# Performance work log

Hardware: AMD Instinct MI355X
Metric: run time of the kernel (lower is better)

Reference implementation:

```python
import jax, jax.numpy as jnp
import numpy as np

N_NODES = 50000
N_EDGES = 800000
F_IN, HID, CLS = 128, 128, 64
DELTA = 3.0


def setup_inputs() -> dict:
    key = jax.random.key(0)
    ks = jax.random.split(key, 16)
    x = jax.random.normal(ks[0], (N_NODES, F_IN), jnp.float32)
    src = jax.random.randint(ks[1], (N_EDGES,), 0, N_NODES, jnp.int64)
    dst = jax.random.randint(ks[2], (N_EDGES,), 0, N_NODES, jnp.int64)
    dims = [(F_IN, HID), (HID, HID), (HID, CLS)]
    inp = {"x": x, "src": src, "dst": dst}
    k = 3
    for i, (din, dout) in enumerate(dims):
        inp[f"M{i}_w"] = jax.random.normal(ks[k], (2 * din, din), jnp.float32) * 0.05; k += 1
        inp[f"M{i}_b"] = jnp.zeros((din,), jnp.float32)
        inp[f"U{i}_w"] = jax.random.normal(ks[k], (10 * din, dout), jnp.float32) * 0.05; k += 1
        inp[f"U{i}_b"] = jnp.zeros((dout,), jnp.float32)
    return inp


def _pna_layer(h, src, dst, deg, logd, Mw, Mb, Uw, Ub):
    # message: per-edge linear on concat(src feat, dst feat)  [E, 2*din] @ [2*din, din]
    msg = jnp.concatenate([h[src], h[dst]], axis=1) @ Mw + Mb  # [E, din]
    n = h.shape[0]
    cnt = deg[:, None]                                          # [N, 1]
    has_nbr = cnt > 0
    mean = jax.ops.segment_sum(msg, dst, num_segments=n) / jnp.maximum(cnt, 1.0)
    mn = jax.ops.segment_min(msg, dst, num_segments=n)
    mx = jax.ops.segment_max(msg, dst, num_segments=n)
    mn = jnp.where(has_nbr, mn, 0.0)
    mx = jnp.where(has_nbr, mx, 0.0)
    agg = jnp.concatenate([mean, mn, mx], axis=1)               # [N, 3*din]
    amp = (logd / DELTA)[:, None]                               # amplification scaler
    att = (DELTA / jnp.maximum(logd, 1e-6))[:, None]            # attenuation scaler
    h_neigh = jnp.concatenate([agg, agg * amp, agg * att], axis=1)  # [N, 9*din]
    return jnp.concatenate([h, h_neigh], axis=1) @ Uw + Ub      # [N, dout]


def reference(x, src, dst, M0_w, M0_b, U0_w, U0_b, M1_w, M1_b, U1_w, U1_b, M2_w, M2_b, U2_w, U2_b):
    n = x.shape[0]
    deg = jax.ops.segment_sum(jnp.ones_like(dst, dtype=x.dtype), dst, num_segments=n)
    logd = jnp.log(deg + 1.0)
    params = [(M0_w, M0_b, U0_w, U0_b), (M1_w, M1_b, U1_w, U1_b), (M2_w, M2_b, U2_w, U2_b)]
    h = x
    for i, (Mw, Mb, Uw, Ub) in enumerate(params):
        h = _pna_layer(h, src, dst, deg, logd, Mw, Mb, Uw, Ub)
        if i != len(params) - 1:
            h = jax.nn.relu(h)
    return h
```

## Files before the change

kernel.cpp:

```cpp
#include <hip/hip_runtime.h>
#include <math.h>

#define N_NODES 50000
#define N_EDGES 800000
#define DIN 128
#define NB_SCAN ((N_NODES + 255) / 256)

typedef unsigned short u16;
typedef unsigned int u32;
typedef short short8 __attribute__((ext_vector_type(8)));
typedef float f32x4 __attribute__((ext_vector_type(4)));

__device__ __forceinline__ u16 f2bf(float x) {
  u32 u = __float_as_uint(x);
  u32 r = (u + 0x7FFFu + ((u >> 16) & 1u)) >> 16;
  return (u16)r;
}
__device__ __forceinline__ float bf2f(u16 h) { return __uint_as_float(((u32)h) << 16); }
__device__ __forceinline__ u32 pack2bf(float x, float y) {
  return (u32)f2bf(x) | ((u32)f2bf(y) << 16);
}

__device__ __forceinline__ f32x4 mfma_bf16(short8 a, short8 b, f32x4 c) {
  return __builtin_amdgcn_mfma_f32_16x16x32_bf16(a, b, c, 0, 0, 0);
}

__device__ __forceinline__ void g2l16(const void* g, void* l) {
  __builtin_amdgcn_global_load_lds(
      (const __attribute__((address_space(1))) u32*)g,
      (__attribute__((address_space(3))) u32*)l, 16, 0, 0);
}

#define SWZ(row, byt) ((row) * 128 + ((byt) ^ (((row) & 7) << 4)))


__global__ void k_deg(const int* __restrict__ dst, int* __restrict__ deg) {
  int e = blockIdx.x * blockDim.x + threadIdx.x;
  if (e < N_EDGES) atomicAdd(&deg[dst[e]], 1);
}

__global__ void k_scan_local(const int* __restrict__ deg, int* __restrict__ excl,
                             int* __restrict__ bsum) {
  __shared__ int sm[256];
  int tid = threadIdx.x;
  int i = blockIdx.x * 256 + tid;
  int v = (i < N_NODES) ? deg[i] : 0;
  sm[tid] = v;
  __syncthreads();
  for (int off = 1; off < 256; off <<= 1) {
    int t = (tid >= off) ? sm[tid - off] : 0;
    __syncthreads();
    sm[tid] += t;
    __syncthreads();
  }
  if (i < N_NODES) excl[i] = sm[tid] - v;
  if (tid == 255) bsum[blockIdx.x] = sm[255];
}

__global__ void k_scan_bsum(const int* __restrict__ bsum, int* __restrict__ boff,
                            int* __restrict__ row_off) {
  __shared__ int sm[256];
  int tid = threadIdx.x;
  int v = (tid < NB_SCAN) ? bsum[tid] : 0;
  sm[tid] = v;
  __syncthreads();
  for (int off = 1; off < 256; off <<= 1) {
    int t = (tid >= off) ? sm[tid - off] : 0;
    __syncthreads();
    sm[tid] += t;
    __syncthreads();
  }
  if (tid < NB_SCAN) boff[tid] = sm[tid] - v;
  if (tid == 255) row_off[N_NODES] = sm[255];
}

__global__ void k_scan_add(const int* __restrict__ excl, const int* __restrict__ boff,
                           int* __restrict__ row_off) {
  int i = blockIdx.x * 256 + threadIdx.x;
  if (i < N_NODES) row_off[i] = excl[i] + boff[i >> 8];
}

__global__ void k_node_init(const int* __restrict__ deg, const int* __restrict__ row_off,
                            int* __restrict__ cursor, float* __restrict__ amp,
                            float* __restrict__ att) {
  int v = blockIdx.x * blockDim.x + threadIdx.x;
  if (v >= N_NODES) return;
  cursor[v] = row_off[v];
  float d = (float)deg[v];
  float logd = logf(d + 1.0f);
  amp[v] = logd / 3.0f;
  att[v] = 3.0f / fmaxf(logd, 1e-6f);
}

__global__ void k_fill(const int* __restrict__ src, const int* __restrict__ dst,
                       int* __restrict__ cursor, int* __restrict__ nbr) {
  int e = blockIdx.x * blockDim.x + threadIdx.x;
  if (e >= N_EDGES) return;
  int slot = atomicAdd(&cursor[dst[e]], 1);
  nbr[slot] = src[e];
}


__global__ void k_prep_ab(const float* __restrict__ Mw, const float* __restrict__ Mb,
                          u16* __restrict__ Th, u16* __restrict__ Tl,
                          float* __restrict__ bias_ab) {
  int j = blockIdx.x;
  int k = threadIdx.x;
  float w = (j < 128) ? Mw[k * 128 + j] : Mw[(128 + k) * 128 + (j - 128)];
  u16 hi = f2bf(w);
  u16 lo = f2bf(w - bf2f(hi));
  Th[j * 128 + k] = hi;
  Tl[j * 128 + k] = lo;
  if (k == 0) bias_ab[j] = (j < 128) ? 0.f : Mb[j - 128];
}

__global__ void k_prep_u(const float* __restrict__ Uw, u16* __restrict__ Th,
                         u16* __restrict__ Tl, int Nout) {
  int k = blockIdx.x * 256 + threadIdx.x;
  int j = blockIdx.y;
  int p = blockIdx.z;
  if (p > 0 && k < 128) return;
  int srow = (p == 0) ? k : 512 + 384 * (p - 1) + (k - 128);
  float w = Uw[(size_t)srow * Nout + j];
  u16 hi = f2bf(w);
  u16 lo = f2bf(w - bf2f(hi));
  size_t idx = ((size_t)p * Nout + j) * 512 + k;
  Th[idx] = hi;
  Tl[idx] = lo;
}


__global__ void k_pack_x(const float* __restrict__ x, u16* __restrict__ Xh,
                         u16* __restrict__ Xl) {
  int i = blockIdx.x * 256 + threadIdx.x;
  if (i >= N_NODES * DIN) return;
  int g = i >> 7, c = i & 127;
  float v = x[i];
  u16 hi = f2bf(v);
  Xh[(size_t)g * 512 + c] = hi;
  Xl[(size_t)g * 128 + c] = f2bf(v - bf2f(hi));
}


__global__ __launch_bounds__(256, 3) void k_ab_gemm(
    const u16* __restrict__ Xh, const u16* __restrict__ Xl,
    const u16* __restrict__ WTh, const u16* __restrict__ WTl,
    const float* __restrict__ bias, u16* __restrict__ ABa, float* __restrict__ ABb) {
  __shared__ __align__(16) u16 Ah[128 * 64];
  __shared__ __align__(16) u16 Al[128 * 64];
  __shared__ __align__(16) u16 Bh[64 * 64];
  __shared__ __align__(16) u16 Bl[64 * 64];

  const int tid = threadIdx.x;
  const int row0 = blockIdx.x * 128;
  const int col0 = blockIdx.y * 64;
  const int lane = tid & 63;
  const int wave = tid >> 6;
  const int wrow = (wave >> 1) * 64;
  const int wcol = (wave & 1) * 32;

  f32x4 acc[4][2];
  const f32x4 zero4 = {0.f, 0.f, 0.f, 0.f};
#pragma unroll
  for (int i = 0; i < 4; ++i)
#pragma unroll
    for (int n = 0; n < 2; ++n) acc[i][n] = zero4;

  for (int k0 = 0; k0 < 128; k0 += 64) {
    __syncthreads();
#pragma unroll
    for (int r = 0; r < 4; ++r) {
      int op = r * 256 + tid;
      int m = op >> 3, ch = op & 7;
      int chx = ch ^ (m & 7);
      int g = row0 + m;
      if (g >= N_NODES) g = N_NODES - 1;
      g2l16(Xh + (size_t)g * 512 + k0 + chx * 8, (char*)Ah + op * 16);
      g2l16(Xl + (size_t)g * 128 + k0 + chx * 8, (char*)Al + op * 16);
    }
#pragma unroll
    for (int r = 0; r < 2; ++r) {
      int op = r * 256 + tid;
      int c = op >> 3, sl = op & 7;
      int slx = sl ^ (c & 7);
      g2l16(WTh + (size_t)(col0 + c) * 128 + k0 + slx * 8, (char*)Bh + op * 16);
      g2l16(WTl + (size_t)(col0 + c) * 128 + k0 + slx * 8, (char*)Bl + op * 16);
    }
    __syncthreads();
#pragma unroll
    for (int kk = 0; kk < 2; ++kk) {
      const int kb = kk * 64 + (lane >> 4) * 16;
      short8 a_h[4], a_l[4];
#pragma unroll
      for (int i = 0; i < 4; ++i) {
        int rr = wrow + i * 16 + (lane & 15);
        a_h[i] = *(const short8*)((const char*)Ah + SWZ(rr, kb));
        a_l[i] = *(const short8*)((const char*)Al + SWZ(rr, kb));
      }
#pragma unroll
      for (int n = 0; n < 2; ++n) {
        int cc = wcol + n * 16 + (lane & 15);
        short8 b_h = *(const short8*)((const char*)Bh + SWZ(cc, kb));
        short8 b_l = *(const short8*)((const char*)Bl + SWZ(cc, kb));
#pragma unroll
        for (int i = 0; i < 4; ++i) {
          acc[i][n] = mfma_bf16(a_h[i], b_h, acc[i][n]);
          acc[i][n] = mfma_bf16(a_h[i], b_l, acc[i][n]);
          acc[i][n] = mfma_bf16(a_l[i], b_h, acc[i][n]);
        }
      }
    }
  }
#pragma unroll
  for (int i = 0; i < 4; ++i) {
#pragma unroll
    for (int n = 0; n < 2; ++n) {
      int gr0 = row0 + wrow + i * 16 + (lane >> 4) * 4;
      int gc = col0 + wcol + n * 16 + (lane & 15);
#pragma unroll
      for (int q = 0; q < 4; ++q) {
        int gr = gr0 + q;
        if (gr >= N_NODES) continue;
        float v = acc[i][n][q];
        if (gc < 128) ABa[(size_t)gr * 128 + gc] = f2bf(v);
        else ABb[(size_t)gr * 128 + (gc - 128)] = v + bias[gc];
      }
    }
  }
}


template <int BN, int LAST>
__global__ __launch_bounds__(256, 3) void k_u_fused(
    const u16* __restrict__ Xh, const u16* __restrict__ Xl,
    const u16* __restrict__ UTh, const u16* __restrict__ UTl,
    const float* __restrict__ Ub, const float* __restrict__ amp,
    const float* __restrict__ att, u16* __restrict__ XhW, u16* __restrict__ XlW,
    float* __restrict__ outF, int Nout) {
  constexpr int NREP = BN / 32;
  constexpr int BE = BN * 64;
  constexpr int L1E = 16384 + 2 * BE;
  constexpr int L2E = 8192 + 4 * BE;
  constexpr int LDSE = (L1E > L2E) ? L1E : L2E;
  __shared__ __align__(16) u16 LDS[LDSE];
  u16* Ah  = LDS;
  u16* Al  = LDS + 8192;
  u16* B0h = LDS + 16384;
  u16* B0l = LDS + 16384 + BE;
  u16* B1h = LDS + 8192;
  u16* B1l = LDS + 8192 + BE;
  u16* B2h = LDS + 8192 + 2 * BE;
  u16* B2l = LDS + 8192 + 3 * BE;

  const int tid = threadIdx.x;
  const int row0 = blockIdx.x * 128;
  const int col0 = blockIdx.y * BN;
  const int lane = tid & 63;
  const int wave = tid >> 6;
  const int wrow = (wave >> 1) * 64;
  const int wcol = (wave & 1) * (BN / 2);

  const u16* U0h = UTh + (size_t)col0 * 512;
  const u16* U0l = UTl + (size_t)col0 * 512;
  const u16* U1h = UTh + (size_t)(Nout + col0) * 512;
  const u16* U1l = UTl + (size_t)(Nout + col0) * 512;
  const u16* U2h = UTh + (size_t)(2 * Nout + col0) * 512;
  const u16* U2l = UTl + (size_t)(2 * Nout + col0) * 512;

  f32x4 acc_t[4][NREP], acc_p1[4][NREP], acc_p2[4][NREP];
  const f32x4 zero4 = {0.f, 0.f, 0.f, 0.f};
#pragma unroll
  for (int i = 0; i < 4; ++i)
#pragma unroll
    for (int n = 0; n < NREP; ++n) {
      acc_t[i][n] = zero4; acc_p1[i][n] = zero4; acc_p2[i][n] = zero4;
    }

  for (int k0 = 0; k0 < 512; k0 += 64) {
    const bool hstep = (k0 < 128);
    __syncthreads();
#pragma unroll
    for (int r = 0; r < 4; ++r) {
      int op = r * 256 + tid;
      int m = op >> 3, ch = op & 7;
      int chx = ch ^ (m & 7);
      int g = row0 + m;
      if (g >= N_NODES) g = N_NODES - 1;
      g2l16(Xh + (size_t)g * 512 + k0 + chx * 8, (char*)Ah + op * 16);
      if (hstep) g2l16(Xl + (size_t)g * 128 + k0 + chx * 8, (char*)Al + op * 16);
    }
#pragma unroll
    for (int r = 0; r < NREP; ++r) {
      int op = r * 256 + tid;
      int c = op >> 3, sl = op & 7;
      int slx = sl ^ (c & 7);
      g2l16(U0h + (size_t)c * 512 + k0 + slx * 8, (char*)B0h + op * 16);
      g2l16(U0l + (size_t)c * 512 + k0 + slx * 8, (char*)B0l + op * 16);
    }
    __syncthreads();
#pragma unroll
    for (int kk = 0; kk < 2; ++kk) {
      const int kb = kk * 64 + (lane >> 4) * 16;
      short8 a_h[4], a_l[4];
#pragma unroll
      for (int i = 0; i < 4; ++i) {
        int rr = wrow + i * 16 + (lane & 15);
        a_h[i] = *(const short8*)((const char*)Ah + SWZ(rr, kb));
        if (hstep) a_l[i] = *(const short8*)((const char*)Al + SWZ(rr, kb));
      }
#pragma unroll
      for (int n = 0; n < NREP; ++n) {
        int cc = wcol + n * 16 + (lane & 15);
        short8 b_h = *(const short8*)((const char*)B0h + SWZ(cc, kb));
        short8 b_l = *(const short8*)((const char*)B0l + SWZ(cc, kb));
#pragma unroll
        for (int i = 0; i < 4; ++i) {
          acc_t[i][n] = mfma_bf16(a_h[i], b_h, acc_t[i][n]);
          acc_t[i][n] = mfma_bf16(a_h[i], b_l, acc_t[i][n]);
          if (hstep) acc_t[i][n] = mfma_bf16(a_l[i], b_h, acc_t[i][n]);
        }
      }
    }
  }

  for (int k0 = 128; k0 < 512; k0 += 64) {
    __syncthreads();
#pragma unroll
    for (int r = 0; r < 4; ++r) {
      int op = r * 256 + tid;
      int m = op >> 3, ch = op & 7;
      int chx = ch ^ (m & 7);
      int g = row0 + m;
      if (g >= N_NODES) g = N_NODES - 1;
      g2l16(Xh + (size_t)g * 512 + k0 + chx * 8, (char*)Ah + op * 16);
    }
#pragma unroll
    for (int r = 0; r < NREP; ++r) {
      int op = r * 256 + tid;
      int c = op >> 3, sl = op & 7;
      int slx = sl ^ (c & 7);
      size_t so = (size_t)c * 512 + k0 + slx * 8;
      g2l16(U1h + so, (char*)B1h + op * 16);
      g2l16(U1l + so, (char*)B1l + op * 16);
      g2l16(U2h + so, (char*)B2h + op * 16);
      g2l16(U2l + so, (char*)B2l + op * 16);
    }
    __syncthreads();
#pragma unroll
    for (int kk = 0; kk < 2; ++kk) {
      const int kb = kk * 64 + (lane >> 4) * 16;
      short8 a_h[4];
#pragma unroll
      for (int i = 0; i < 4; ++i) {
        int rr = wrow + i * 16 + (lane & 15);
        a_h[i] = *(const short8*)((const char*)Ah + SWZ(rr, kb));
      }
#pragma unroll
      for (int n = 0; n < NREP; ++n) {
        int cc = wcol + n * 16 + (lane & 15);
        short8 b1h = *(const short8*)((const char*)B1h + SWZ(cc, kb));
        short8 b1l = *(const short8*)((const char*)B1l + SWZ(cc, kb));
        short8 b2h = *(const short8*)((const char*)B2h + SWZ(cc, kb));
        short8 b2l = *(const short8*)((const char*)B2l + SWZ(cc, kb));
#pragma unroll
        for (int i = 0; i < 4; ++i) {
          acc_p1[i][n] = mfma_bf16(a_h[i], b1h, acc_p1[i][n]);
          acc_p1[i][n] = mfma_bf16(a_h[i], b1l, acc_p1[i][n]);
          acc_p2[i][n] = mfma_bf16(a_h[i], b2h, acc_p2[i][n]);
          acc_p2[i][n] = mfma_bf16(a_h[i], b2l, acc_p2[i][n]);
        }
      }
    }
  }

#pragma unroll
  for (int i = 0; i < 4; ++i) {
    int gr0 = row0 + wrow + i * 16 + (lane >> 4) * 4;
    f32x4 a1 = *(const f32x4*)(amp + gr0);
    f32x4 a2 = *(const f32x4*)(att + gr0);
#pragma unroll
    for (int n = 0; n < NREP; ++n) {
      int gc = col0 + wcol + n * 16 + (lane & 15);
      float b = Ub[gc];
#pragma unroll
      for (int q = 0; q < 4; ++q) {
        int gr = gr0 + q;
        if (gr >= N_NODES) continue;
        float v = acc_t[i][n][q] + a1[q] * acc_p1[i][n][q] + a2[q] * acc_p2[i][n][q] + b;
        if (LAST) {
          outF[(size_t)gr * 64 + gc] = v;
        } else {
          float t = fmaxf(v, 0.f);
          u16 hi = f2bf(t);
          XhW[(size_t)gr * 512 + gc] = hi;
          XlW[(size_t)gr * 128 + gc] = f2bf(t - bf2f(hi));
        }
      }
    }
  }
}


__global__ __launch_bounds__(256) void k_agg(const u16* __restrict__ ABa,
                                             const float* __restrict__ ABb,
                                             const int* __restrict__ row_off,
                                             const int* __restrict__ nbr,
                                             u16* __restrict__ XhDst) {
  int v = blockIdx.x * 4 + (threadIdx.x >> 6);
  int lane = threadIdx.x & 63;
  if (v >= N_NODES) return;
  int beg = row_off[v], end = row_off[v + 1];
  const u32* A32 = (const u32*)ABa;
  float sx = 0.f, sy = 0.f;
  float mnx = 3.4e38f, mny = 3.4e38f;
  float mxx = -3.4e38f, mxy = -3.4e38f;
  int i = beg;
#define ACC(w)                                              \
  {                                                         \
    float ax = bf2f((u16)(w)), ay = bf2f((u16)((w) >> 16)); \
    sx += ax; sy += ay;                                     \
    mnx = fminf(mnx, ax); mny = fminf(mny, ay);             \
    mxx = fmaxf(mxx, ax); mxy = fmaxf(mxy, ay);             \
  }
  for (; i + 4 <= end; i += 4) {
    int s0 = nbr[i], s1 = nbr[i + 1], s2 = nbr[i + 2], s3 = nbr[i + 3];
    u32 w0 = A32[(size_t)s0 * 64 + lane];
    u32 w1 = A32[(size_t)s1 * 64 + lane];
    u32 w2 = A32[(size_t)s2 * 64 + lane];
    u32 w3 = A32[(size_t)s3 * 64 + lane];
    ACC(w0) ACC(w1) ACC(w2) ACC(w3)
  }
  for (; i < end; ++i) {
    u32 w = A32[(size_t)nbr[i] * 64 + lane];
    ACC(w)
  }
#undef ACC
  int d = end - beg;
  int c = lane * 2;
  float2 b = *(const float2*)&ABb[(size_t)v * 128 + c];
  float mex, mey, mix, miy, max_, may_;
  if (d > 0) {
    float inv = 1.f / (float)d;
    mex = sx * inv + b.x; mey = sy * inv + b.y;
    mix = mnx + b.x; miy = mny + b.y;
    max_ = mxx + b.x; may_ = mxy + b.y;
  } else {
    mex = mey = mix = miy = max_ = may_ = 0.f;
  }
  u16* xr = XhDst + (size_t)v * 512 + 128 + c;
  *(u32*)(xr)       = pack2bf(mex, mey);
  *(u32*)(xr + 128) = pack2bf(mix, miy);
  *(u32*)(xr + 256) = pack2bf(max_, may_);
}


extern "C" void kernel_launch(void* const* d_in, const int* in_sizes, int n_in,
                              void* d_out, int out_size, void* d_ws, size_t ws_size,
                              hipStream_t stream) {
  const float* x   = (const float*)d_in[0];
  const int*   src = (const int*)d_in[1];
  const int*   dst = (const int*)d_in[2];
  const float* Mw[3] = {(const float*)d_in[3], (const float*)d_in[7],  (const float*)d_in[11]};
  const float* Mb[3] = {(const float*)d_in[4], (const float*)d_in[8],  (const float*)d_in[12]};
  const float* Uw[3] = {(const float*)d_in[5], (const float*)d_in[9],  (const float*)d_in[13]};
  const float* Ub[3] = {(const float*)d_in[6], (const float*)d_in[10], (const float*)d_in[14]};
  float* out = (float*)d_out;

  char* ws = (char*)d_ws;
  size_t o = 0;
  auto alloc = [&](size_t bytes) -> char* {
    o = (o + 255) & ~(size_t)255;
    char* p = ws + o;
    o += bytes;
    return p;
  };
  int*   deg_i   = (int*)alloc((size_t)N_NODES * 4);
  int*   row_off = (int*)alloc((size_t)(N_NODES + 1) * 4);
  int*   excl    = (int*)alloc((size_t)N_NODES * 4);
  int*   bsum    = (int*)alloc((size_t)NB_SCAN * 4);
  int*   boff    = (int*)alloc((size_t)NB_SCAN * 4);
  int*   cursor  = (int*)alloc((size_t)N_NODES * 4);
  float* amp     = (float*)alloc((size_t)N_NODES * 4);
  float* att     = (float*)alloc((size_t)N_NODES * 4);
  int*   nbr     = (int*)alloc((size_t)N_EDGES * 4);
  u16*   Xh0     = (u16*)alloc((size_t)N_NODES * 512 * 2);
  u16*   Xl0     = (u16*)alloc((size_t)N_NODES * 128 * 2);
  u16*   Xh1     = (u16*)alloc((size_t)N_NODES * 512 * 2);
  u16*   Xl1     = (u16*)alloc((size_t)N_NODES * 128 * 2);
  u16*   ABa     = (u16*)alloc((size_t)N_NODES * 128 * 2);
  float* ABb     = (float*)alloc((size_t)N_NODES * 128 * 4);
  u16*   WabTh[3]; u16* WabTl[3]; float* bias_ab[3];
  u16*   UTh[3];   u16* UTl[3];
  const int Nouts[3] = {128, 128, 64};
  for (int L = 0; L < 3; ++L) {
    WabTh[L] = (u16*)alloc((size_t)256 * 128 * 2);
    WabTl[L] = (u16*)alloc((size_t)256 * 128 * 2);
    bias_ab[L] = (float*)alloc(256 * 4);
    UTh[L] = (u16*)alloc((size_t)3 * Nouts[L] * 512 * 2);
    UTl[L] = (u16*)alloc((size_t)3 * Nouts[L] * 512 * 2);
  }

  hipMemsetAsync(deg_i, 0, (size_t)N_NODES * 4, stream);
  k_deg<<<(N_EDGES + 255) / 256, 256, 0, stream>>>(dst, deg_i);
  k_scan_local<<<NB_SCAN, 256, 0, stream>>>(deg_i, excl, bsum);
  k_scan_bsum<<<1, 256, 0, stream>>>(bsum, boff, row_off);
  k_scan_add<<<NB_SCAN, 256, 0, stream>>>(excl, boff, row_off);
  k_node_init<<<(N_NODES + 255) / 256, 256, 0, stream>>>(deg_i, row_off, cursor, amp, att);
  k_fill<<<(N_EDGES + 255) / 256, 256, 0, stream>>>(src, dst, cursor, nbr);

  for (int L = 0; L < 3; ++L) {
    k_prep_ab<<<256, 128, 0, stream>>>(Mw[L], Mb[L], WabTh[L], WabTl[L], bias_ab[L]);
    k_prep_u<<<dim3(2, Nouts[L], 3), 256, 0, stream>>>(Uw[L], UTh[L], UTl[L], Nouts[L]);
  }
  k_pack_x<<<(N_NODES * DIN + 255) / 256, 256, 0, stream>>>(x, Xh0, Xl0);

  const int MT = (N_NODES + 127) / 128;
  u16* XhIn[3] = {Xh0, Xh1, Xh0};
  u16* XlIn[3] = {Xl0, Xl1, Xl0};
  u16* XhOut[3] = {Xh1, Xh0, nullptr};
  u16* XlOut[3] = {Xl1, Xl0, nullptr};

  for (int L = 0; L < 3; ++L) {
    k_ab_gemm<<<dim3(MT, 4), 256, 0, stream>>>(XhIn[L], XlIn[L], WabTh[L], WabTl[L],
                                               bias_ab[L], ABa, ABb);
    k_agg<<<(N_NODES + 3) / 4, 256, 0, stream>>>(ABa, ABb, row_off, nbr, XhIn[L]);
    if (L < 2) {
      k_u_fused<64, 0><<<dim3(MT, 2), 256, 0, stream>>>(
          XhIn[L], XlIn[L], UTh[L], UTl[L], Ub[L], amp, att,
          XhOut[L], XlOut[L], nullptr, Nouts[L]);
    } else {
      k_u_fused<32, 1><<<dim3(MT, 2), 256, 0, stream>>>(
          XhIn[L], XlIn[L], UTh[L], UTl[L], Ub[L], amp, att,
          nullptr, nullptr, out, Nouts[L]);
    }
  }
}
```

Before: 601.2 us.

## Swap grid axes, merge U-GEMM k-loops, and vectorize aggregation per 16-lane node group

Result: faster. 568.4 us (-5.5%).

```diff
diff --git a/kernel.cpp b/kernel.cpp
--- a/kernel.cpp
+++ b/kernel.cpp
@@ -152,8 +152,8 @@
   __shared__ __align__(16) u16 Bl[64 * 64];
 
   const int tid = threadIdx.x;
-  const int row0 = blockIdx.x * 128;
-  const int col0 = blockIdx.y * 64;
+  const int row0 = blockIdx.y * 128;
+  const int col0 = blockIdx.x * 64;
   const int lane = tid & 63;
   const int wave = tid >> 6;
   const int wrow = (wave >> 1) * 64;
@@ -231,7 +231,7 @@
 
 
 template <int BN, int LAST>
-__global__ __launch_bounds__(256, 3) void k_u_fused(
+__global__ __launch_bounds__(256, 2) void k_u_fused(
     const u16* __restrict__ Xh, const u16* __restrict__ Xl,
     const u16* __restrict__ UTh, const u16* __restrict__ UTl,
     const float* __restrict__ Ub, const float* __restrict__ amp,
@@ -239,22 +239,20 @@
     float* __restrict__ outF, int Nout) {
   constexpr int NREP = BN / 32;
   constexpr int BE = BN * 64;
-  constexpr int L1E = 16384 + 2 * BE;
-  constexpr int L2E = 8192 + 4 * BE;
-  constexpr int LDSE = (L1E > L2E) ? L1E : L2E;
+  constexpr int LDSE = 8192 + 2 * BE + ((4 * BE > 8192) ? 4 * BE : 8192);
   __shared__ __align__(16) u16 LDS[LDSE];
   u16* Ah  = LDS;
-  u16* Al  = LDS + 8192;
-  u16* B0h = LDS + 16384;
-  u16* B0l = LDS + 16384 + BE;
-  u16* B1h = LDS + 8192;
-  u16* B1l = LDS + 8192 + BE;
-  u16* B2h = LDS + 8192 + 2 * BE;
-  u16* B2l = LDS + 8192 + 3 * BE;
+  u16* B0h = LDS + 8192;
+  u16* B0l = LDS + 8192 + BE;
+  u16* B1h = LDS + 8192 + 2 * BE;
+  u16* B1l = LDS + 8192 + 3 * BE;
+  u16* B2h = LDS + 8192 + 4 * BE;
+  u16* B2l = LDS + 8192 + 5 * BE;
+  u16* Al  = LDS + 8192 + 2 * BE;
 
   const int tid = threadIdx.x;
-  const int row0 = blockIdx.x * 128;
-  const int col0 = blockIdx.y * BN;
+  const int row0 = blockIdx.y * 128;
+  const int col0 = blockIdx.x * BN;
   const int lane = tid & 63;
   const int wave = tid >> 6;
   const int wrow = (wave >> 1) * 64;
@@ -294,8 +292,15 @@
       int op = r * 256 + tid;
       int c = op >> 3, sl = op & 7;
       int slx = sl ^ (c & 7);
-      g2l16(U0h + (size_t)c * 512 + k0 + slx * 8, (char*)B0h + op * 16);
-      g2l16(U0l + (size_t)c * 512 + k0 + slx * 8, (char*)B0l + op * 16);
+      size_t so = (size_t)c * 512 + k0 + slx * 8;
+      g2l16(U0h + so, (char*)B0h + op * 16);
+      g2l16(U0l + so, (char*)B0l + op * 16);
+      if (!hstep) {
+        g2l16(U1h + so, (char*)B1h + op * 16);
+        g2l16(U1l + so, (char*)B1l + op * 16);
+        g2l16(U2h + so, (char*)B2h + op * 16);
+        g2l16(U2l + so, (char*)B2l + op * 16);
+      }
     }
     __syncthreads();
 #pragma unroll
@@ -311,63 +316,26 @@
 #pragma unroll
       for (int n = 0; n < NREP; ++n) {
         int cc = wcol + n * 16 + (lane & 15);
-        short8 b_h = *(const short8*)((const char*)B0h + SWZ(cc, kb));
-        short8 b_l = *(const short8*)((const char*)B0l + SWZ(cc, kb));
+        short8 b0h = *(const short8*)((const char*)B0h + SWZ(cc, kb));
+        short8 b0l = *(const short8*)((const char*)B0l + SWZ(cc, kb));
 #pragma unroll
         for (int i = 0; i < 4; ++i) {
-          acc_t[i][n] = mfma_bf16(a_h[i], b_h, acc_t[i][n]);
-          acc_t[i][n] = mfma_bf16(a_h[i], b_l, acc_t[i][n]);
-          if (hstep) acc_t[i][n] = mfma_bf16(a_l[i], b_h, acc_t[i][n]);
+          acc_t[i][n] = mfma_bf16(a_h[i], b0h, acc_t[i][n]);
+          acc_t[i][n] = mfma_bf16(a_h[i], b0l, acc_t[i][n]);
+          if (hstep) acc_t[i][n] = mfma_bf16(a_l[i], b0h, acc_t[i][n]);
         }
-      }
-    }
-  }
-
-  for (int k0 = 128; k0 < 512; k0 += 64) {
-    __syncthreads();
-#pragma unroll
-    for (int r = 0; r < 4; ++r) {
-      int op = r * 256 + tid;
-      int m = op >> 3, ch = op & 7;
-      int chx = ch ^ (m & 7);
-      int g = row0 + m;
-      if (g >= N_NODES) g = N_NODES - 1;
-      g2l16(Xh + (size_t)g * 512 + k0 + chx * 8, (char*)Ah + op * 16);
-    }
-#pragma unroll
-    for (int r = 0; r < NREP; ++r) {
-      int op = r * 256 + tid;
-      int c = op >> 3, sl = op & 7;
-      int slx = sl ^ (c & 7);
-      size_t so = (size_t)c * 512 + k0 + slx * 8;
-      g2l16(U1h + so, (char*)B1h + op * 16);
-      g2l16(U1l + so, (char*)B1l + op * 16);
-      g2l16(U2h + so, (char*)B2h + op * 16);
-      g2l16(U2l + so, (char*)B2l + op * 16);
-    }
-    __syncthreads();
-#pragma unroll
-    for (int kk = 0; kk < 2; ++kk) {
-      const int kb = kk * 64 + (lane >> 4) * 16;
-      short8 a_h[4];
-#pragma unroll
-      for (int i = 0; i < 4; ++i) {
-        int rr = wrow + i * 16 + (lane & 15);
-        a_h[i] = *(const short8*)((const char*)Ah + SWZ(rr, kb));
-      }
-#pragma unroll
-      for (int n = 0; n < NREP; ++n) {
-        int cc = wcol + n * 16 + (lane & 15);
-        short8 b1h = *(const short8*)((const char*)B1h + SWZ(cc, kb));
-        short8 b1l = *(const short8*)((const char*)B1l + SWZ(cc, kb));
-        short8 b2h = *(const short8*)((const char*)B2h + SWZ(cc, kb));
-        short8 b2l = *(const short8*)((const char*)B2l + SWZ(cc, kb));
-#pragma unroll
-        for (int i = 0; i < 4; ++i) {
-          acc_p1[i][n] = mfma_bf16(a_h[i], b1h, acc_p1[i][n]);
-          acc_p1[i][n] = mfma_bf16(a_h[i], b1l, acc_p1[i][n]);
-          acc_p2[i][n] = mfma_bf16(a_h[i], b2h, acc_p2[i][n]);
-          acc_p2[i][n] = mfma_bf16(a_h[i], b2l, acc_p2[i][n]);
+        if (!hstep) {
+          short8 b1h = *(const short8*)((const char*)B1h + SWZ(cc, kb));
+          short8 b1l = *(const short8*)((const char*)B1l + SWZ(cc, kb));
+          short8 b2h = *(const short8*)((const char*)B2h + SWZ(cc, kb));
+          short8 b2l = *(const short8*)((const char*)B2l + SWZ(cc, kb));
+#pragma unroll
+          for (int i = 0; i < 4; ++i) {
+            acc_p1[i][n] = mfma_bf16(a_h[i], b1h, acc_p1[i][n]);
+            acc_p1[i][n] = mfma_bf16(a_h[i], b1l, acc_p1[i][n]);
+            acc_p2[i][n] = mfma_bf16(a_h[i], b2h, acc_p2[i][n]);
+            acc_p2[i][n] = mfma_bf16(a_h[i], b2l, acc_p2[i][n]);
+          }
         }
       }
     }
@@ -406,51 +374,55 @@
                                              const int* __restrict__ row_off,
                                              const int* __restrict__ nbr,
                                              u16* __restrict__ XhDst) {
-  int v = blockIdx.x * 4 + (threadIdx.x >> 6);
+  int wv = blockIdx.x * 4 + (threadIdx.x >> 6);
   int lane = threadIdx.x & 63;
+  int grp = lane >> 4;
+  int sub = lane & 15;
+  int v = wv * 4 + grp;
   if (v >= N_NODES) return;
   int beg = row_off[v], end = row_off[v + 1];
-  const u32* A32 = (const u32*)ABa;
-  float sx = 0.f, sy = 0.f;
-  float mnx = 3.4e38f, mny = 3.4e38f;
-  float mxx = -3.4e38f, mxy = -3.4e38f;
-  int i = beg;
-#define ACC(w)                                              \
-  {                                                         \
-    float ax = bf2f((u16)(w)), ay = bf2f((u16)((w) >> 16)); \
-    sx += ax; sy += ay;                                     \
-    mnx = fminf(mnx, ax); mny = fminf(mny, ay);             \
-    mxx = fmaxf(mxx, ax); mxy = fmaxf(mxy, ay);             \
-  }
-  for (; i + 4 <= end; i += 4) {
-    int s0 = nbr[i], s1 = nbr[i + 1], s2 = nbr[i + 2], s3 = nbr[i + 3];
-    u32 w0 = A32[(size_t)s0 * 64 + lane];
-    u32 w1 = A32[(size_t)s1 * 64 + lane];
-    u32 w2 = A32[(size_t)s2 * 64 + lane];
-    u32 w3 = A32[(size_t)s3 * 64 + lane];
-    ACC(w0) ACC(w1) ACC(w2) ACC(w3)
-  }
-  for (; i < end; ++i) {
-    u32 w = A32[(size_t)nbr[i] * 64 + lane];
-    ACC(w)
-  }
-#undef ACC
+  const uint4* A16 = (const uint4*)ABa;
+  float s[8], mn[8], mx[8];
+#pragma unroll
+  for (int c = 0; c < 8; ++c) { s[c] = 0.f; mn[c] = 3.4e38f; mx[c] = -3.4e38f; }
+  for (int i = beg; i < end; ++i) {
+    int sidx = nbr[i];
+    uint4 w = A16[(size_t)sidx * 16 + sub];
+    u32 ww[4] = {w.x, w.y, w.z, w.w};
+#pragma unroll
+    for (int j = 0; j < 4; ++j) {
+      float ax = bf2f((u16)ww[j]), ay = bf2f((u16)(ww[j] >> 16));
+      s[2 * j] += ax; s[2 * j + 1] += ay;
+      mn[2 * j] = fminf(mn[2 * j], ax); mn[2 * j + 1] = fminf(mn[2 * j + 1], ay);
+      mx[2 * j] = fmaxf(mx[2 * j], ax); mx[2 * j + 1] = fmaxf(mx[2 * j + 1], ay);
+    }
+  }
   int d = end - beg;
-  int c = lane * 2;
-  float2 b = *(const float2*)&ABb[(size_t)v * 128 + c];
-  float mex, mey, mix, miy, max_, may_;
+  float bb[8];
+  {
+    f32x4 b0 = *(const f32x4*)(ABb + (size_t)v * 128 + sub * 8);
+    f32x4 b1 = *(const f32x4*)(ABb + (size_t)v * 128 + sub * 8 + 4);
+#pragma unroll
+    for (int c = 0; c < 4; ++c) { bb[c] = b0[c]; bb[4 + c] = b1[c]; }
+  }
+  uint4 wm, wn, wx;
+  u32* pm = &wm.x; u32* pn = &wn.x; u32* px = &wx.x;
   if (d > 0) {
     float inv = 1.f / (float)d;
-    mex = sx * inv + b.x; mey = sy * inv + b.y;
-    mix = mnx + b.x; miy = mny + b.y;
-    max_ = mxx + b.x; may_ = mxy + b.y;
+#pragma unroll
+    for (int j = 0; j < 4; ++j) {
+      pm[j] = pack2bf(s[2 * j] * inv + bb[2 * j], s[2 * j + 1] * inv + bb[2 * j + 1]);
+      pn[j] = pack2bf(mn[2 * j] + bb[2 * j], mn[2 * j + 1] + bb[2 * j + 1]);
+      px[j] = pack2bf(mx[2 * j] + bb[2 * j], mx[2 * j + 1] + bb[2 * j + 1]);
+    }
   } else {
-    mex = mey = mix = miy = max_ = may_ = 0.f;
-  }
-  u16* xr = XhDst + (size_t)v * 512 + 128 + c;
-  *(u32*)(xr)       = pack2bf(mex, mey);
-  *(u32*)(xr + 128) = pack2bf(mix, miy);
-  *(u32*)(xr + 256) = pack2bf(max_, may_);
+#pragma unroll
+    for (int j = 0; j < 4; ++j) { pm[j] = 0u; pn[j] = 0u; px[j] = 0u; }
+  }
+  uint4* xr = (uint4*)(XhDst + (size_t)v * 512);
+  xr[16 + sub] = wm;
+  xr[32 + sub] = wn;
+  xr[48 + sub] = wx;
 }
 
 
@@ -521,15 +493,15 @@
   u16* XlOut[3] = {Xl1, Xl0, nullptr};
 
   for (int L = 0; L < 3; ++L) {
-    k_ab_gemm<<<dim3(MT, 4), 256, 0, stream>>>(XhIn[L], XlIn[L], WabTh[L], WabTl[L],
+    k_ab_gemm<<<dim3(4, MT), 256, 0, stream>>>(XhIn[L], XlIn[L], WabTh[L], WabTl[L],
                                                bias_ab[L], ABa, ABb);
-    k_agg<<<(N_NODES + 3) / 4, 256, 0, stream>>>(ABa, ABb, row_off, nbr, XhIn[L]);
+    k_agg<<<(N_NODES + 15) / 16, 256, 0, stream>>>(ABa, ABb, row_off, nbr, XhIn[L]);
     if (L < 2) {
-      k_u_fused<64, 0><<<dim3(MT, 2), 256, 0, stream>>>(
+      k_u_fused<64, 0><<<dim3(2, MT), 256, 0, stream>>>(
           XhIn[L], XlIn[L], UTh[L], UTl[L], Ub[L], amp, att,
           XhOut[L], XlOut[L], nullptr, Nouts[L]);
     } else {
-      k_u_fused<32, 1><<<dim3(MT, 2), 256, 0, stream>>>(
+      k_u_fused<32, 1><<<dim3(2, MT), 256, 0, stream>>>(
           XhIn[L], XlIn[L], UTh[L], UTl[L], Ub[L], amp, att,
           nullptr, nullptr, out, Nouts[L]);
     }
```
